# Performance work log

Measured on AMD Instinct MI355X. Metric: run time of the kernel, lower is better.

## Reference

```python
import jax, jax.numpy as jnp
import numpy as np

SEARCH_SIZE = 21
BLOCK_SIZE = 4


def _inter_prediction(im1, im2, search_size=SEARCH_SIZE, block_size=BLOCK_SIZE):
    # im1, im2: [B, 1, H, W]; returns [B, 1, H, W]
    B, C, H, W = im1.shape
    p = search_size // 2
    s2 = search_size * search_size
    im2_pad = jnp.pad(im2, ((0, 0), (0, 0), (p, p), (p, p)))
    # All SxS shifted views of im2, stacked on channel dim: [B, S^2, H, W].
    # Channel k = (i, j) row-major corresponds to im2_pad[:, :, i:i+H, j:j+W],
    # matching the torch double loop (note: output is permutation-invariant
    # over shifts anyway since weights are derived from the same tensor).
    nbr = jax.lax.conv_general_dilated_patches(
        im2_pad, (search_size, search_size), (1, 1), 'VALID')
    diff = jnp.abs(im1 - nbr)  # broadcast [B,1,H,W] against [B,S^2,H,W]
    h, w = H // block_size, W // block_size
    # avg_pool2d with kernel=stride=block_size via reshape-mean
    vol = diff.reshape(B, s2, h, block_size, w, block_size).mean(axis=(3, 5))
    idx = jax.nn.softmax(-100.0 * vol, axis=1)  # [B, S^2, h, w]
    # repeat_interleave(block_size) along both spatial dims
    idx_full = jnp.broadcast_to(
        idx[:, :, :, None, :, None],
        (B, s2, h, block_size, w, block_size)).reshape(B, s2, H, W)
    return jnp.sum(idx_full * nbr, axis=1, keepdims=True)


def setup_inputs() -> dict:
    key = jax.random.key(0)
    k1, k2 = jax.random.split(key)
    im1 = jax.random.normal(k1, (2, 1, 256, 256), dtype=jnp.float32)
    im2 = jax.random.normal(k2, (2, 1, 256, 256), dtype=jnp.float32)
    return {"im1": im1, "im2": im2}


def reference(im1, im2):
    return _inter_prediction(im1, im2)
```

## Files before the change

kernel.cpp:

```cpp
#include <hip/hip_runtime.h>
#include <math.h>


#define HH 256
#define WW 256
#define PAD 10
#define WINR 28
#define WSTR 29
#define LDSN (WINR * WSTR)

__global__ __launch_bounds__(256) void pred_kernel(
    const float* __restrict__ im1, const float* __restrict__ im2,
    float* __restrict__ out) {
  __shared__ float win[LDSN];

  const int tid = threadIdx.x;
  const int T = blockIdx.x;
  const int b = T >> 10;
  const int rem = T & 1023;
  const int tr = rem >> 5;
  const int tc = rem & 31;
  const float* im2b = im2 + b * (HH * WW);

  for (int e = tid; e < LDSN; e += 256) {
    int wr = e / WSTR;
    int wc = e - wr * WSTR;
    int gr = tr * 8 + wr - PAD;
    int gc = tc * 8 + wc - PAD;
    float v = 0.f;
    if ((unsigned)gr < HH && (unsigned)gc < WW) v = im2b[gr * WW + gc];
    win[e] = v;
  }
  __syncthreads();

  const int wave = tid >> 6;
  const int lane = tid & 63;
  const int by = tr * 2 + (wave >> 1);
  const int bx = tc * 2 + (wave & 1);
  const int wbase = ((wave >> 1) * 4) * WSTR + (wave & 1) * 4;

  float a[16];
  const float* im1b = im1 + b * (HH * WW) + (by * 4) * WW + bx * 4;
#pragma unroll
  for (int dy = 0; dy < 4; ++dy) {
    const float4 r = *reinterpret_cast<const float4*>(im1b + dy * WW);
    a[dy * 4 + 0] = r.x; a[dy * 4 + 1] = r.y;
    a[dy * 4 + 2] = r.z; a[dy * 4 + 3] = r.w;
  }

  const int i = lane / 3;
  const int j0 = (lane - i * 3) * 7;
  const int base = wbase + i * WSTR + j0;
  float w[40];
#pragma unroll
  for (int dy = 0; dy < 4; ++dy)
#pragma unroll
    for (int c = 0; c < 10; ++c) w[dy * 10 + c] = win[base + dy * WSTR + c];

  float sad[7];
#pragma unroll
  for (int t = 0; t < 7; ++t) {
    float s0 = 0.f, s1 = 0.f, s2 = 0.f, s3 = 0.f;
#pragma unroll
    for (int dy = 0; dy < 4; ++dy) {
      s0 += fabsf(a[dy * 4 + 0] - w[dy * 10 + t + 0]);
      s1 += fabsf(a[dy * 4 + 1] - w[dy * 10 + t + 1]);
      s2 += fabsf(a[dy * 4 + 2] - w[dy * 10 + t + 2]);
      s3 += fabsf(a[dy * 4 + 3] - w[dy * 10 + t + 3]);
    }
    sad[t] = (s0 + s1) + (s2 + s3);
  }
  if (lane == 63) {
#pragma unroll
    for (int t = 0; t < 7; ++t) sad[t] = 3.0e38f;
  }

  float m = sad[0];
#pragma unroll
  for (int t = 1; t < 7; ++t) m = fminf(m, sad[t]);
#pragma unroll
  for (int off = 32; off; off >>= 1) m = fminf(m, __shfl_xor(m, off, 64));

  const float cc = 9.016844005556021f;
  float l = 0.f;
  float o[16];
#pragma unroll
  for (int t = 0; t < 16; ++t) o[t] = 0.f;
#pragma unroll
  for (int t = 0; t < 7; ++t) {
    const float p = __builtin_amdgcn_exp2f(cc * (m - sad[t]));
    l += p;
#pragma unroll
    for (int dy = 0; dy < 4; ++dy)
#pragma unroll
      for (int dx = 0; dx < 4; ++dx)
        o[dy * 4 + dx] = __builtin_fmaf(p, w[dy * 10 + t + dx], o[dy * 4 + dx]);
  }

  float r8[8];
  {
    const bool up = (lane & 32) != 0;
#pragma unroll
    for (int q = 0; q < 8; ++q) {
      const float send = up ? o[q] : o[q + 8];
      const float recv = __shfl_xor(send, 32, 64);
      r8[q] = (up ? o[q + 8] : o[q]) + recv;
    }
  }
  float r4[4];
  {
    const bool up = (lane & 16) != 0;
#pragma unroll
    for (int q = 0; q < 4; ++q) {
      const float send = up ? r8[q] : r8[q + 4];
      const float recv = __shfl_xor(send, 16, 64);
      r4[q] = (up ? r8[q + 4] : r8[q]) + recv;
    }
  }
  float r2[2];
  {
    const bool up = (lane & 8) != 0;
#pragma unroll
    for (int q = 0; q < 2; ++q) {
      const float send = up ? r4[q] : r4[q + 2];
      const float recv = __shfl_xor(send, 8, 64);
      r2[q] = (up ? r4[q + 2] : r4[q]) + recv;
    }
  }
  float r1;
  {
    const bool up = (lane & 4) != 0;
    const float send = up ? r2[0] : r2[1];
    const float recv = __shfl_xor(send, 4, 64);
    r1 = (up ? r2[1] : r2[0]) + recv;
  }
  r1 += __shfl_xor(r1, 2, 64);
  r1 += __shfl_xor(r1, 1, 64);

#pragma unroll
  for (int off = 32; off; off >>= 1) l += __shfl_xor(l, off, 64);
  const float rinv = __builtin_amdgcn_rcpf(l);

  if ((lane & 3) == 0) {
    const int t = lane >> 2;
    out[b * (HH * WW) + (by * 4 + (t >> 2)) * WW + bx * 4 + (t & 3)] =
        r1 * rinv;
  }
}

extern "C" void kernel_launch(void* const* d_in, const int* in_sizes, int n_in,
                              void* d_out, int out_size, void* d_ws, size_t ws_size,
                              hipStream_t stream) {
  const float* im1 = (const float*)d_in[0];
  const float* im2 = (const float*)d_in[1];
  float* out = (float*)d_out;
  const int B = in_sizes[0] / (HH * WW);
  pred_kernel<<<B * 1024, 256, 0, stream>>>(im1, im2, out);
}
```

Measured before the change: 65.33 us.

## Transpose LDS window into parity copies and use packed float2 math

Stores the im2 search window in LDS column-major, with a second copy shifted by one row, so each lane can read row pairs as aligned 8-byte float2 loads whatever the parity of its row. SAD and weighted-sum accumulation then run on two-wide vectors, aiming to use packed FP32 instructions (pk_add/pk_fma) and halve the LDS read instruction count. In exchange the LDS footprint and the store traffic during tile fill roughly double, and stores are now strided.

```diff
diff --git a/kernel.cpp b/kernel.cpp
--- a/kernel.cpp
+++ b/kernel.cpp
@@ -2,17 +2,21 @@
 #include <math.h>
 
 
+typedef float v2f __attribute__((ext_vector_type(2)));
+
 #define HH 256
 #define WW 256
 #define PAD 10
-#define WINR 28
-#define WSTR 29
-#define LDSN (WINR * WSTR)
+#define NR 28
+#define NC 28
+#define CSTR 30
+#define COPY (NC * CSTR)
+#define LDSN (2 * COPY)
 
 __global__ __launch_bounds__(256) void pred_kernel(
     const float* __restrict__ im1, const float* __restrict__ im2,
     float* __restrict__ out) {
-  __shared__ float win[LDSN];
+  __shared__ __attribute__((aligned(16))) float win2[LDSN];
 
   const int tid = threadIdx.x;
   const int T = blockIdx.x;
@@ -22,14 +26,15 @@
   const int tc = rem & 31;
   const float* im2b = im2 + b * (HH * WW);
 
-  for (int e = tid; e < LDSN; e += 256) {
-    int wr = e / WSTR;
-    int wc = e - wr * WSTR;
-    int gr = tr * 8 + wr - PAD;
-    int gc = tc * 8 + wc - PAD;
+  for (int e = tid; e < NR * NC; e += 256) {
+    const int r = e / NC;
+    const int c = e - r * NC;
+    const int gr = tr * 8 + r - PAD;
+    const int gc = tc * 8 + c - PAD;
     float v = 0.f;
     if ((unsigned)gr < HH && (unsigned)gc < WW) v = im2b[gr * WW + gc];
-    win[e] = v;
+    win2[c * CSTR + r] = v;
+    if (r >= 1) win2[COPY + c * CSTR + (r - 1)] = v;
   }
   __syncthreads();
 
@@ -37,38 +42,50 @@
   const int lane = tid & 63;
   const int by = tr * 2 + (wave >> 1);
   const int bx = tc * 2 + (wave & 1);
-  const int wbase = ((wave >> 1) * 4) * WSTR + (wave & 1) * 4;
 
-  float a[16];
-  const float* im1b = im1 + b * (HH * WW) + (by * 4) * WW + bx * 4;
-#pragma unroll
-  for (int dy = 0; dy < 4; ++dy) {
-    const float4 r = *reinterpret_cast<const float4*>(im1b + dy * WW);
-    a[dy * 4 + 0] = r.x; a[dy * 4 + 1] = r.y;
-    a[dy * 4 + 2] = r.z; a[dy * 4 + 3] = r.w;
+  v2f a2[4][2];
+  {
+    const float* im1b = im1 + b * (HH * WW) + (by * 4) * WW + bx * 4;
+    const float4 r0 = *reinterpret_cast<const float4*>(im1b + 0 * WW);
+    const float4 r1 = *reinterpret_cast<const float4*>(im1b + 1 * WW);
+    const float4 r2 = *reinterpret_cast<const float4*>(im1b + 2 * WW);
+    const float4 r3 = *reinterpret_cast<const float4*>(im1b + 3 * WW);
+    a2[0][0] = (v2f){r0.x, r1.x}; a2[1][0] = (v2f){r0.y, r1.y};
+    a2[2][0] = (v2f){r0.z, r1.z}; a2[3][0] = (v2f){r0.w, r1.w};
+    a2[0][1] = (v2f){r2.x, r3.x}; a2[1][1] = (v2f){r2.y, r3.y};
+    a2[2][1] = (v2f){r2.z, r3.z}; a2[3][1] = (v2f){r2.w, r3.w};
   }
 
   const int i = lane / 3;
   const int j0 = (lane - i * 3) * 7;
-  const int base = wbase + i * WSTR + j0;
-  float w[40];
+  const int ir = i + (wave >> 1) * 4;
+  const int jc = j0 + (wave & 1) * 4;
+  const int par = ir & 1;
+  const int q0 = ir - par;
+  const int baseIdx = par * COPY + jc * CSTR + q0;
+
+  v2f w2[10][2];
 #pragma unroll
-  for (int dy = 0; dy < 4; ++dy)
+  for (int c = 0; c < 10; ++c) {
 #pragma unroll
-    for (int c = 0; c < 10; ++c) w[dy * 10 + c] = win[base + dy * WSTR + c];
+    for (int rp = 0; rp < 2; ++rp)
+      w2[c][rp] = *reinterpret_cast<const v2f*>(
+          &win2[baseIdx + c * CSTR + 2 * rp]);
+  }
 
   float sad[7];
 #pragma unroll
   for (int t = 0; t < 7; ++t) {
-    float s0 = 0.f, s1 = 0.f, s2 = 0.f, s3 = 0.f;
+    v2f acc = (v2f){0.f, 0.f};
 #pragma unroll
-    for (int dy = 0; dy < 4; ++dy) {
-      s0 += fabsf(a[dy * 4 + 0] - w[dy * 10 + t + 0]);
-      s1 += fabsf(a[dy * 4 + 1] - w[dy * 10 + t + 1]);
-      s2 += fabsf(a[dy * 4 + 2] - w[dy * 10 + t + 2]);
-      s3 += fabsf(a[dy * 4 + 3] - w[dy * 10 + t + 3]);
+    for (int c = 0; c < 4; ++c) {
+#pragma unroll
+      for (int rp = 0; rp < 2; ++rp) {
+        const v2f d = a2[c][rp] - w2[t + c][rp];
+        acc += __builtin_elementwise_max(d, -d);
+      }
     }
-    sad[t] = (s0 + s1) + (s2 + s3);
+    sad[t] = acc.x + acc.y;
   }
   if (lane == 63) {
 #pragma unroll
@@ -82,20 +99,33 @@
   for (int off = 32; off; off >>= 1) m = fminf(m, __shfl_xor(m, off, 64));
 
   const float cc = 9.016844005556021f;
+  const float cm = cc * m;
   float l = 0.f;
+  v2f o2[4][2];
+#pragma unroll
+  for (int c = 0; c < 4; ++c)
+#pragma unroll
+    for (int rp = 0; rp < 2; ++rp) o2[c][rp] = (v2f){0.f, 0.f};
+#pragma unroll
+  for (int t = 0; t < 7; ++t) {
+    const float p = __builtin_amdgcn_exp2f(__builtin_fmaf(-cc, sad[t], cm));
+    l += p;
+    const v2f pv = (v2f){p, p};
+#pragma unroll
+    for (int c = 0; c < 4; ++c)
+#pragma unroll
+      for (int rp = 0; rp < 2; ++rp)
+        o2[c][rp] += pv * w2[t + c][rp];
+  }
+
   float o[16];
 #pragma unroll
-  for (int t = 0; t < 16; ++t) o[t] = 0.f;
+  for (int c = 0; c < 4; ++c)
 #pragma unroll
-  for (int t = 0; t < 7; ++t) {
-    const float p = __builtin_amdgcn_exp2f(cc * (m - sad[t]));
-    l += p;
-#pragma unroll
-    for (int dy = 0; dy < 4; ++dy)
-#pragma unroll
-      for (int dx = 0; dx < 4; ++dx)
-        o[dy * 4 + dx] = __builtin_fmaf(p, w[dy * 10 + t + dx], o[dy * 4 + dx]);
-  }
+    for (int rp = 0; rp < 2; ++rp) {
+      o[(2 * rp + 0) * 4 + c] = o2[c][rp].x;
+      o[(2 * rp + 1) * 4 + c] = o2[c][rp].y;
+    }
 
   float r8[8];
   {
```

New measurement: 64.34 us. Within noise of the previous version (-1.5%).
